# Performance work log

Hardware: AMD Instinct MI355X
Metric: run time of the kernel (lower is better)

The kernel has to match this reference:

```python
import jax, jax.numpy as jnp
import numpy as np

TOP_K = 2
NORM_TOPK_PROB = True


def setup_inputs() -> dict:
    key = jax.random.key(0)
    k1, k2, k3, k4 = jax.random.split(key, 4)
    B, S, H = 1, 1024, 2048
    E, I = 16, 768
    hidden_states = jax.random.normal(k1, (B, S, H), dtype=jnp.float32)
    # 0.02 init scale keeps router logits / activations in a realistic range
    gate_w = jax.random.normal(k2, (E, H), dtype=jnp.float32) * 0.02
    w1 = jax.random.normal(k3, (E, 2 * I, H), dtype=jnp.float32) * 0.02  # [gate; up] stacked
    w2 = jax.random.normal(k4, (E, H, I), dtype=jnp.float32) * 0.02
    return {"hidden_states": hidden_states, "gate_w": gate_w, "w1": w1, "w2": w2}


def reference(hidden_states, gate_w, w1, w2):
    B, S, H = hidden_states.shape
    E = gate_w.shape[0]
    I = w2.shape[2]
    x = hidden_states.reshape(-1, H)  # [T, H]

    # Router
    router_logits = x @ gate_w.T  # [T, E]
    probs = jax.nn.softmax(router_logits.astype(jnp.float32), axis=-1)
    topk_w, topk_ids = jax.lax.top_k(probs, TOP_K)  # [T, K]
    if NORM_TOPK_PROB:
        topk_w = topk_w / jnp.sum(topk_w, axis=-1, keepdims=True)
    topk_w = topk_w.astype(x.dtype)

    # combine[t, e] = sum_k topk_w[t, k] * 1[topk_ids[t, k] == e]
    combine = jnp.sum(jax.nn.one_hot(topk_ids, E, dtype=x.dtype) * topk_w[..., None], axis=1)  # [T, E]

    def expert(w1_e, w2_e):
        h = x @ w1_e.T                      # [T, 2I]
        act = jax.nn.silu(h[:, :I]) * h[:, I:]  # fused SiLU-and-mul
        return act @ w2_e.T                 # [T, H]

    y_all = jax.vmap(expert)(w1, w2)        # [E, T, H]
    out = jnp.einsum('te,eth->th', combine, y_all)  # weighted scatter-sum over experts
    return out, router_logits
```

## Files before the change

### kernel.cpp

```cpp
#include <hip/hip_runtime.h>
#include <hip/hip_bf16.h>


#define T_TOK 1024
#define HDIM  2048
#define NEXP  16
#define IDIM  768
#define CAP   192
#define BK    64

typedef __attribute__((ext_vector_type(8))) short  short8_t;
typedef __attribute__((ext_vector_type(4))) float  f32x4_t;

static __device__ __forceinline__ unsigned short f2bf(float f) {
  unsigned u = __float_as_uint(f);
  u += 0x7FFFu + ((u >> 16) & 1u);
  return (unsigned short)(u >> 16);
}
static __device__ __forceinline__ float bf2f(unsigned short h) {
  return __uint_as_float(((unsigned)h) << 16);
}
static __device__ __forceinline__ void cvt_store4(unsigned short* dst, float4 v) {
  ushort4 u;
  u.x = f2bf(v.x); u.y = f2bf(v.y); u.z = f2bf(v.z); u.w = f2bf(v.w);
  *(ushort4*)dst = u;
}

__global__ __launch_bounds__(256) void moe_router(
    const float* __restrict__ x, const float* __restrict__ gw,
    float* __restrict__ logits_out, int* __restrict__ cnt,
    int* __restrict__ tok, float* __restrict__ wl) {
  const int t = blockIdx.x;
  const int tid = threadIdx.x;
  const int lane = tid & 63, wid = tid >> 6;
  const float4* xv = (const float4*)(x + (size_t)t * HDIM);
  float4 v0 = xv[tid * 2], v1 = xv[tid * 2 + 1];
  float acc[NEXP];
#pragma unroll
  for (int e = 0; e < NEXP; ++e) {
    const float4* gv = (const float4*)(gw + (size_t)e * HDIM);
    float4 g0 = gv[tid * 2], g1 = gv[tid * 2 + 1];
    acc[e] = v0.x * g0.x + v0.y * g0.y + v0.z * g0.z + v0.w * g0.w +
             v1.x * g1.x + v1.y * g1.y + v1.z * g1.z + v1.w * g1.w;
  }
#pragma unroll
  for (int e = 0; e < NEXP; ++e)
#pragma unroll
    for (int off = 32; off; off >>= 1) acc[e] += __shfl_xor(acc[e], off, 64);
  __shared__ float red[4][NEXP];
  if (lane == 0)
#pragma unroll
    for (int e = 0; e < NEXP; ++e) red[wid][e] = acc[e];
  __syncthreads();
  if (tid < NEXP) {
    float s = red[0][tid] + red[1][tid] + red[2][tid] + red[3][tid];
    logits_out[(size_t)t * NEXP + tid] = s;
    red[0][tid] = s;
  }
  __syncthreads();
  if (tid == 0) {
    int e1 = -1, e2 = -1;
    float l1 = -1e30f, l2 = -1e30f;
#pragma unroll
    for (int e = 0; e < NEXP; ++e) {
      float v = red[0][e];
      if (v > l1)      { l2 = l1; e2 = e1; l1 = v; e1 = e; }
      else if (v > l2) { l2 = v;  e2 = e; }
    }
    float wa = 1.f / (1.f + __expf(l2 - l1));
    float wb = 1.f - wa;
    int p1 = atomicAdd(&cnt[e1], 1);
    if (p1 < CAP) { tok[e1 * CAP + p1] = t; wl[e1 * CAP + p1] = wa; }
    int p2 = atomicAdd(&cnt[e2], 1);
    if (p2 < CAP) { tok[e2 * CAP + p2] = t; wl[e2 * CAP + p2] = wb; }
  }
}

__global__ __launch_bounds__(256, 3) void moe_stage_a(
    const float* __restrict__ x, const float* __restrict__ w1,
    const int* __restrict__ cnt, const int* __restrict__ tok,
    unsigned short* __restrict__ h_ws) {
  int bx = blockIdx.x;
  const int ks = bx & 1; bx >>= 1;
  const int mt = bx & 1; bx >>= 1;
  const int nt = bx % 24;
  const int e  = bx / 24;
  int ne = cnt[e]; if (ne > CAP) ne = CAP;
  if (mt * 128 >= ne) return;

  __shared__ unsigned short As[128][BK + 8];
  __shared__ unsigned short Bs[64][BK + 8];
  __shared__ int toks[128];
  const int tid = threadIdx.x;
  if (tid < 128) {
    int idx = mt * 128 + tid;
    toks[tid] = tok[e * CAP + (idx < ne ? idx : 0)];
  }
  __syncthreads();

  const int k0 = ks * (HDIM / 2);
  const float* aB[8];
#pragma unroll
  for (int i = 0; i < 8; ++i) {
    int c = tid + 256 * i, r = c >> 4, c4 = c & 15;
    aB[i] = x + (size_t)toks[r] * HDIM + k0 + c4 * 4;
  }
  const float* w1e = w1 + ((size_t)e * (2 * IDIM) + nt * 64) * HDIM + k0;
  const float* bB[4];
#pragma unroll
  for (int i = 0; i < 4; ++i) {
    int c = tid + 256 * i, r = c >> 4, c4 = c & 15;
    bB[i] = w1e + (size_t)r * HDIM + c4 * 4;
  }

  float4 aR[8], bR[4];
#pragma unroll
  for (int i = 0; i < 8; ++i) aR[i] = *(const float4*)(aB[i]);
#pragma unroll
  for (int i = 0; i < 4; ++i) bR[i] = *(const float4*)(bB[i]);

  const int lane = tid & 63, wv = tid >> 6;
  const int wr = wv >> 1, wc = wv & 1;
  const int quad = lane >> 4, lr = lane & 15;
  f32x4_t acc[4][2] = {};

  for (int kk = 0; kk < HDIM / 2; kk += BK) {
#pragma unroll
    for (int i = 0; i < 8; ++i) {
      int c = tid + 256 * i;
      cvt_store4(&As[c >> 4][(c & 15) * 4], aR[i]);
    }
#pragma unroll
    for (int i = 0; i < 4; ++i) {
      int c = tid + 256 * i;
      cvt_store4(&Bs[c >> 4][(c & 15) * 4], bR[i]);
    }
    __syncthreads();
    if (kk + BK < HDIM / 2) {
      int kn = kk + BK;
#pragma unroll
      for (int i = 0; i < 8; ++i) aR[i] = *(const float4*)(aB[i] + kn);
#pragma unroll
      for (int i = 0; i < 4; ++i) bR[i] = *(const float4*)(bB[i] + kn);
    }
    short8_t a[2][4], b[2][2];
#pragma unroll
    for (int k2 = 0; k2 < 2; ++k2) {
#pragma unroll
      for (int i = 0; i < 4; ++i)
        a[k2][i] = *(const short8_t*)&As[wr * 64 + i * 16 + lr][k2 * 32 + quad * 8];
#pragma unroll
      for (int j = 0; j < 2; ++j)
        b[k2][j] = *(const short8_t*)&Bs[wc * 32 + j * 16 + lr][k2 * 32 + quad * 8];
    }
#pragma unroll
    for (int k2 = 0; k2 < 2; ++k2)
#pragma unroll
      for (int i = 0; i < 4; ++i)
#pragma unroll
        for (int j = 0; j < 2; ++j)
          acc[i][j] = __builtin_amdgcn_mfma_f32_16x16x32_bf16(
              a[k2][i], b[k2][j], acc[i][j], 0, 0, 0);
    __syncthreads();
  }

  unsigned short* hp = h_ws + ((size_t)ks * NEXP + e) * CAP * (2 * IDIM);
#pragma unroll
  for (int i = 0; i < 4; ++i) {
    int mb = mt * 128 + wr * 64 + i * 16;
    if (mb >= CAP) continue;
#pragma unroll
    for (int j = 0; j < 2; ++j) {
      int ng = nt * 64 + wc * 32 + j * 16 + lr;
#pragma unroll
      for (int rr = 0; rr < 4; ++rr) {
        int mg = mb + quad * 4 + rr;
        hp[(size_t)mg * (2 * IDIM) + ng] = f2bf(acc[i][j][rr]);
      }
    }
  }
}

__global__ __launch_bounds__(256) void moe_merge(
    const unsigned short* __restrict__ h_ws, unsigned short* __restrict__ act) {
  const size_t half = (size_t)NEXP * CAP * (2 * IDIM);
  int c = blockIdx.x * 256 + threadIdx.x;
  int row = c / (IDIM / 4);
  int c4  = c % (IDIM / 4);
  size_t gb = (size_t)row * (2 * IDIM) + c4 * 4;
  ushort4 g0 = *(const ushort4*)(h_ws + gb);
  ushort4 g1 = *(const ushort4*)(h_ws + half + gb);
  ushort4 u0 = *(const ushort4*)(h_ws + gb + IDIM);
  ushort4 u1 = *(const ushort4*)(h_ws + half + gb + IDIM);
  float g, u;
  ushort4 o;
  g = bf2f(g0.x) + bf2f(g1.x); u = bf2f(u0.x) + bf2f(u1.x);
  o.x = f2bf(g / (1.f + __expf(-g)) * u);
  g = bf2f(g0.y) + bf2f(g1.y); u = bf2f(u0.y) + bf2f(u1.y);
  o.y = f2bf(g / (1.f + __expf(-g)) * u);
  g = bf2f(g0.z) + bf2f(g1.z); u = bf2f(u0.z) + bf2f(u1.z);
  o.z = f2bf(g / (1.f + __expf(-g)) * u);
  g = bf2f(g0.w) + bf2f(g1.w); u = bf2f(u0.w) + bf2f(u1.w);
  o.w = f2bf(g / (1.f + __expf(-g)) * u);
  *(ushort4*)(act + (size_t)row * IDIM + c4 * 4) = o;
}

__global__ __launch_bounds__(256, 2) void moe_stage_b(
    const unsigned short* __restrict__ act, const float* __restrict__ w2,
    const int* __restrict__ cnt, const int* __restrict__ tok,
    const float* __restrict__ wl, float* __restrict__ out) {
  int bx = blockIdx.x;
  const int mt = bx & 1; bx >>= 1;
  const int nt = bx & 31;
  const int e  = bx >> 5;
  int ne = cnt[e]; if (ne > CAP) ne = CAP;
  if (mt * 128 >= ne) return;

  __shared__ unsigned short As[128][BK + 8];
  __shared__ unsigned short Bs[64][BK + 8];
  __shared__ int   toks[128];
  __shared__ float wts[128];
  const int tid = threadIdx.x;
  if (tid < 128) {
    int idx = mt * 128 + tid;
    bool v = idx < ne;
    toks[tid] = tok[e * CAP + (v ? idx : 0)];
    wts[tid]  = v ? wl[e * CAP + idx] : 0.f;
  }
  __syncthreads();

  const unsigned short* actb = act + ((size_t)e * CAP + mt * 128) * IDIM;
  const unsigned short* aB[8];
#pragma unroll
  for (int i = 0; i < 8; ++i) {
    int c = tid + 256 * i, r = c >> 4, c4 = c & 15;
    aB[i] = actb + (size_t)r * IDIM + c4 * 4;
  }
  const float* w2e = w2 + ((size_t)e * HDIM + nt * 64) * IDIM;
  const float* bB[4];
#pragma unroll
  for (int i = 0; i < 4; ++i) {
    int c = tid + 256 * i, r = c >> 4, c4 = c & 15;
    bB[i] = w2e + (size_t)r * IDIM + c4 * 4;
  }

  ushort4 aR[8]; float4 bR[4];
#pragma unroll
  for (int i = 0; i < 8; ++i) aR[i] = *(const ushort4*)(aB[i]);
#pragma unroll
  for (int i = 0; i < 4; ++i) bR[i] = *(const float4*)(bB[i]);

  const int lane = tid & 63, wv = tid >> 6;
  const int wr = wv >> 1, wc = wv & 1;
  const int quad = lane >> 4, lr = lane & 15;
  f32x4_t acc[4][2] = {};

  for (int kk = 0; kk < IDIM; kk += BK) {
#pragma unroll
    for (int i = 0; i < 8; ++i) {
      int c = tid + 256 * i;
      *(ushort4*)&As[c >> 4][(c & 15) * 4] = aR[i];
    }
#pragma unroll
    for (int i = 0; i < 4; ++i) {
      int c = tid + 256 * i;
      cvt_store4(&Bs[c >> 4][(c & 15) * 4], bR[i]);
    }
    __syncthreads();
    if (kk + BK < IDIM) {
      int kn = kk + BK;
#pragma unroll
      for (int i = 0; i < 8; ++i) aR[i] = *(const ushort4*)(aB[i] + kn);
#pragma unroll
      for (int i = 0; i < 4; ++i) bR[i] = *(const float4*)(bB[i] + kn);
    }
    short8_t a[2][4], b[2][2];
#pragma unroll
    for (int k2 = 0; k2 < 2; ++k2) {
#pragma unroll
      for (int i = 0; i < 4; ++i)
        a[k2][i] = *(const short8_t*)&As[wr * 64 + i * 16 + lr][k2 * 32 + quad * 8];
#pragma unroll
      for (int j = 0; j < 2; ++j)
        b[k2][j] = *(const short8_t*)&Bs[wc * 32 + j * 16 + lr][k2 * 32 + quad * 8];
    }
#pragma unroll
    for (int k2 = 0; k2 < 2; ++k2)
#pragma unroll
      for (int i = 0; i < 4; ++i)
#pragma unroll
        for (int j = 0; j < 2; ++j)
          acc[i][j] = __builtin_amdgcn_mfma_f32_16x16x32_bf16(
              a[k2][i], b[k2][j], acc[i][j], 0, 0, 0);
    __syncthreads();
  }

#pragma unroll
  for (int i = 0; i < 4; ++i) {
#pragma unroll
    for (int j = 0; j < 2; ++j) {
      int ng = nt * 64 + wc * 32 + j * 16 + lr;
#pragma unroll
      for (int rr = 0; rr < 4; ++rr) {
        int ml = wr * 64 + i * 16 + quad * 4 + rr;
        atomicAdd(&out[(size_t)toks[ml] * HDIM + ng], acc[i][j][rr] * wts[ml]);
      }
    }
  }
}

extern "C" void kernel_launch(void* const* d_in, const int* in_sizes, int n_in,
                              void* d_out, int out_size, void* d_ws,
                              size_t ws_size, hipStream_t stream) {
  (void)in_sizes; (void)n_in; (void)out_size; (void)ws_size;
  const float* x  = (const float*)d_in[0];
  const float* gw = (const float*)d_in[1];
  const float* w1 = (const float*)d_in[2];
  const float* w2 = (const float*)d_in[3];
  float* out    = (float*)d_out;
  float* logits = out + (size_t)T_TOK * HDIM;

  char* ws = (char*)d_ws;
  int*   cnt = (int*)ws;
  int*   tok = (int*)(ws + 256);
  float* wl  = (float*)(ws + 256 + NEXP * CAP * 4);
  unsigned short* act =
      (unsigned short*)(ws + 25088);
  unsigned short* h_ws =
      (unsigned short*)(ws + 25088 + (size_t)NEXP * CAP * IDIM * 2);

  hipMemsetAsync(cnt, 0, 256, stream);
  hipMemsetAsync(d_out, 0, (size_t)T_TOK * HDIM * sizeof(float), stream);

  moe_router <<<T_TOK, 256, 0, stream>>>(x, gw, logits, cnt, tok, wl);
  moe_stage_a<<<NEXP * 24 * 2 * 2, 256, 0, stream>>>(x, w1, cnt, tok, h_ws);
  moe_merge  <<<NEXP * CAP * IDIM / 4 / 256, 256, 0, stream>>>(h_ws, act);
  moe_stage_b<<<NEXP * 32 * 2, 256, 0, stream>>>(act, w2, cnt, tok, wl, out);
}
```

Baseline: 489.1 us.

## Pre-convert x to bf16, add split-K to both stages, shrink K tile

A new kernel converts x to bf16 once, so stage A no longer loads and converts fp32 activations inside its inner loop. Stage A split-K grows to 4 when the workspace allows it, and the merge kernel sums a variable number of partials. Stage B gains a 2-way split-K that relies on its existing atomic accumulation. Both GEMMs drop to a 32-wide K tile with occupancy hint 4, giving more blocks and fewer registers, at the cost of more barriers, more partial-sum traffic and more atomics.

```diff
diff --git a/kernel.cpp b/kernel.cpp
--- a/kernel.cpp
+++ b/kernel.cpp
@@ -7,7 +7,6 @@
 #define NEXP  16
 #define IDIM  768
 #define CAP   192
-#define BK    64
 
 typedef __attribute__((ext_vector_type(8))) short  short8_t;
 typedef __attribute__((ext_vector_type(4))) float  f32x4_t;
@@ -24,6 +23,13 @@
   ushort4 u;
   u.x = f2bf(v.x); u.y = f2bf(v.y); u.z = f2bf(v.z); u.w = f2bf(v.w);
   *(ushort4*)dst = u;
+}
+
+__global__ __launch_bounds__(256) void cvt_x(
+    const float* __restrict__ x, unsigned short* __restrict__ xb) {
+  int i = blockIdx.x * 256 + threadIdx.x;
+  float4 v = ((const float4*)x)[i];
+  cvt_store4(xb + (size_t)i * 4, v);
 }
 
 __global__ __launch_bounds__(256) void moe_router(
@@ -76,20 +82,20 @@
   }
 }
 
-__global__ __launch_bounds__(256, 3) void moe_stage_a(
-    const float* __restrict__ x, const float* __restrict__ w1,
+__global__ __launch_bounds__(256, 4) void moe_stage_a(
+    const unsigned short* __restrict__ xb, const float* __restrict__ w1,
     const int* __restrict__ cnt, const int* __restrict__ tok,
-    unsigned short* __restrict__ h_ws) {
+    unsigned short* __restrict__ h_ws, int ksa, int kchunk) {
   int bx = blockIdx.x;
-  const int ks = bx & 1; bx >>= 1;
+  const int ks = bx % ksa; bx /= ksa;
   const int mt = bx & 1; bx >>= 1;
   const int nt = bx % 24;
   const int e  = bx / 24;
   int ne = cnt[e]; if (ne > CAP) ne = CAP;
   if (mt * 128 >= ne) return;
 
-  __shared__ unsigned short As[128][BK + 8];
-  __shared__ unsigned short Bs[64][BK + 8];
+  __shared__ unsigned short As[128][40];
+  __shared__ unsigned short Bs[64][40];
   __shared__ int toks[128];
   const int tid = threadIdx.x;
   if (tid < 128) {
@@ -98,69 +104,57 @@
   }
   __syncthreads();
 
-  const int k0 = ks * (HDIM / 2);
-  const float* aB[8];
-#pragma unroll
-  for (int i = 0; i < 8; ++i) {
-    int c = tid + 256 * i, r = c >> 4, c4 = c & 15;
-    aB[i] = x + (size_t)toks[r] * HDIM + k0 + c4 * 4;
+  const int k0 = ks * kchunk;
+  const unsigned short* aB[2];
+  int ar[2], ag[2], br[2], bc[2];
+#pragma unroll
+  for (int i = 0; i < 2; ++i) {
+    int c = tid + 256 * i;
+    ar[i] = c >> 2; ag[i] = c & 3;
+    aB[i] = xb + (size_t)toks[ar[i]] * HDIM + k0 + ag[i] * 8;
+    br[i] = c >> 3; bc[i] = c & 7;
   }
   const float* w1e = w1 + ((size_t)e * (2 * IDIM) + nt * 64) * HDIM + k0;
-  const float* bB[4];
-#pragma unroll
-  for (int i = 0; i < 4; ++i) {
-    int c = tid + 256 * i, r = c >> 4, c4 = c & 15;
-    bB[i] = w1e + (size_t)r * HDIM + c4 * 4;
-  }
-
-  float4 aR[8], bR[4];
-#pragma unroll
-  for (int i = 0; i < 8; ++i) aR[i] = *(const float4*)(aB[i]);
-#pragma unroll
-  for (int i = 0; i < 4; ++i) bR[i] = *(const float4*)(bB[i]);
+  const float* bB[2];
+#pragma unroll
+  for (int i = 0; i < 2; ++i) bB[i] = w1e + (size_t)br[i] * HDIM + bc[i] * 4;
+
+  short8_t aR[2]; float4 bR[2];
+#pragma unroll
+  for (int i = 0; i < 2; ++i) aR[i] = *(const short8_t*)(aB[i]);
+#pragma unroll
+  for (int i = 0; i < 2; ++i) bR[i] = *(const float4*)(bB[i]);
 
   const int lane = tid & 63, wv = tid >> 6;
   const int wr = wv >> 1, wc = wv & 1;
   const int quad = lane >> 4, lr = lane & 15;
   f32x4_t acc[4][2] = {};
 
-  for (int kk = 0; kk < HDIM / 2; kk += BK) {
-#pragma unroll
-    for (int i = 0; i < 8; ++i) {
-      int c = tid + 256 * i;
-      cvt_store4(&As[c >> 4][(c & 15) * 4], aR[i]);
-    }
-#pragma unroll
-    for (int i = 0; i < 4; ++i) {
-      int c = tid + 256 * i;
-      cvt_store4(&Bs[c >> 4][(c & 15) * 4], bR[i]);
-    }
+  for (int kk = 0; kk < kchunk; kk += 32) {
+#pragma unroll
+    for (int i = 0; i < 2; ++i) *(short8_t*)&As[ar[i]][ag[i] * 8] = aR[i];
+#pragma unroll
+    for (int i = 0; i < 2; ++i) cvt_store4(&Bs[br[i]][bc[i] * 4], bR[i]);
     __syncthreads();
-    if (kk + BK < HDIM / 2) {
-      int kn = kk + BK;
-#pragma unroll
-      for (int i = 0; i < 8; ++i) aR[i] = *(const float4*)(aB[i] + kn);
-#pragma unroll
-      for (int i = 0; i < 4; ++i) bR[i] = *(const float4*)(bB[i] + kn);
-    }
-    short8_t a[2][4], b[2][2];
-#pragma unroll
-    for (int k2 = 0; k2 < 2; ++k2) {
-#pragma unroll
-      for (int i = 0; i < 4; ++i)
-        a[k2][i] = *(const short8_t*)&As[wr * 64 + i * 16 + lr][k2 * 32 + quad * 8];
+    if (kk + 32 < kchunk) {
+#pragma unroll
+      for (int i = 0; i < 2; ++i) aR[i] = *(const short8_t*)(aB[i] + kk + 32);
+#pragma unroll
+      for (int i = 0; i < 2; ++i) bR[i] = *(const float4*)(bB[i] + kk + 32);
+    }
+    short8_t a[4], b[2];
+#pragma unroll
+    for (int i = 0; i < 4; ++i)
+      a[i] = *(const short8_t*)&As[wr * 64 + i * 16 + lr][quad * 8];
+#pragma unroll
+    for (int j = 0; j < 2; ++j)
+      b[j] = *(const short8_t*)&Bs[wc * 32 + j * 16 + lr][quad * 8];
+#pragma unroll
+    for (int i = 0; i < 4; ++i)
 #pragma unroll
       for (int j = 0; j < 2; ++j)
-        b[k2][j] = *(const short8_t*)&Bs[wc * 32 + j * 16 + lr][k2 * 32 + quad * 8];
-    }
-#pragma unroll
-    for (int k2 = 0; k2 < 2; ++k2)
-#pragma unroll
-      for (int i = 0; i < 4; ++i)
-#pragma unroll
-        for (int j = 0; j < 2; ++j)
-          acc[i][j] = __builtin_amdgcn_mfma_f32_16x16x32_bf16(
-              a[k2][i], b[k2][j], acc[i][j], 0, 0, 0);
+        acc[i][j] = __builtin_amdgcn_mfma_f32_16x16x32_bf16(
+            a[i], b[j], acc[i][j], 0, 0, 0);
     __syncthreads();
   }
 
@@ -182,42 +176,42 @@
 }
 
 __global__ __launch_bounds__(256) void moe_merge(
-    const unsigned short* __restrict__ h_ws, unsigned short* __restrict__ act) {
-  const size_t half = (size_t)NEXP * CAP * (2 * IDIM);
+    const unsigned short* __restrict__ h_ws, unsigned short* __restrict__ act,
+    int ksa) {
+  const size_t part = (size_t)NEXP * CAP * (2 * IDIM);
   int c = blockIdx.x * 256 + threadIdx.x;
   int row = c / (IDIM / 4);
   int c4  = c % (IDIM / 4);
   size_t gb = (size_t)row * (2 * IDIM) + c4 * 4;
-  ushort4 g0 = *(const ushort4*)(h_ws + gb);
-  ushort4 g1 = *(const ushort4*)(h_ws + half + gb);
-  ushort4 u0 = *(const ushort4*)(h_ws + gb + IDIM);
-  ushort4 u1 = *(const ushort4*)(h_ws + half + gb + IDIM);
-  float g, u;
+  float g[4] = {0.f, 0.f, 0.f, 0.f}, u[4] = {0.f, 0.f, 0.f, 0.f};
+  for (int s = 0; s < ksa; ++s) {
+    ushort4 gs = *(const ushort4*)(h_ws + (size_t)s * part + gb);
+    ushort4 us = *(const ushort4*)(h_ws + (size_t)s * part + gb + IDIM);
+    g[0] += bf2f(gs.x); g[1] += bf2f(gs.y); g[2] += bf2f(gs.z); g[3] += bf2f(gs.w);
+    u[0] += bf2f(us.x); u[1] += bf2f(us.y); u[2] += bf2f(us.z); u[3] += bf2f(us.w);
+  }
   ushort4 o;
-  g = bf2f(g0.x) + bf2f(g1.x); u = bf2f(u0.x) + bf2f(u1.x);
-  o.x = f2bf(g / (1.f + __expf(-g)) * u);
-  g = bf2f(g0.y) + bf2f(g1.y); u = bf2f(u0.y) + bf2f(u1.y);
-  o.y = f2bf(g / (1.f + __expf(-g)) * u);
-  g = bf2f(g0.z) + bf2f(g1.z); u = bf2f(u0.z) + bf2f(u1.z);
-  o.z = f2bf(g / (1.f + __expf(-g)) * u);
-  g = bf2f(g0.w) + bf2f(g1.w); u = bf2f(u0.w) + bf2f(u1.w);
-  o.w = f2bf(g / (1.f + __expf(-g)) * u);
+  o.x = f2bf(g[0] / (1.f + __expf(-g[0])) * u[0]);
+  o.y = f2bf(g[1] / (1.f + __expf(-g[1])) * u[1]);
+  o.z = f2bf(g[2] / (1.f + __expf(-g[2])) * u[2]);
+  o.w = f2bf(g[3] / (1.f + __expf(-g[3])) * u[3]);
   *(ushort4*)(act + (size_t)row * IDIM + c4 * 4) = o;
 }
 
-__global__ __launch_bounds__(256, 2) void moe_stage_b(
+__global__ __launch_bounds__(256, 4) void moe_stage_b(
     const unsigned short* __restrict__ act, const float* __restrict__ w2,
     const int* __restrict__ cnt, const int* __restrict__ tok,
     const float* __restrict__ wl, float* __restrict__ out) {
   int bx = blockIdx.x;
-  const int mt = bx & 1; bx >>= 1;
-  const int nt = bx & 31;
-  const int e  = bx >> 5;
+  const int ks = bx & 1;
+  const int mt = (bx >> 1) & 1;
+  const int nt = (bx >> 2) & 31;
+  const int e  = bx >> 7;
   int ne = cnt[e]; if (ne > CAP) ne = CAP;
   if (mt * 128 >= ne) return;
 
-  __shared__ unsigned short As[128][BK + 8];
-  __shared__ unsigned short Bs[64][BK + 8];
+  __shared__ unsigned short As[128][40];
+  __shared__ unsigned short Bs[64][40];
   __shared__ int   toks[128];
   __shared__ float wts[128];
   const int tid = threadIdx.x;
@@ -229,69 +223,57 @@
   }
   __syncthreads();
 
-  const unsigned short* actb = act + ((size_t)e * CAP + mt * 128) * IDIM;
-  const unsigned short* aB[8];
-#pragma unroll
-  for (int i = 0; i < 8; ++i) {
-    int c = tid + 256 * i, r = c >> 4, c4 = c & 15;
-    aB[i] = actb + (size_t)r * IDIM + c4 * 4;
-  }
-  const float* w2e = w2 + ((size_t)e * HDIM + nt * 64) * IDIM;
-  const float* bB[4];
-#pragma unroll
-  for (int i = 0; i < 4; ++i) {
-    int c = tid + 256 * i, r = c >> 4, c4 = c & 15;
-    bB[i] = w2e + (size_t)r * IDIM + c4 * 4;
-  }
-
-  ushort4 aR[8]; float4 bR[4];
-#pragma unroll
-  for (int i = 0; i < 8; ++i) aR[i] = *(const ushort4*)(aB[i]);
-#pragma unroll
-  for (int i = 0; i < 4; ++i) bR[i] = *(const float4*)(bB[i]);
+  const int k0 = ks * (IDIM / 2);
+  const unsigned short* actb = act + ((size_t)e * CAP + mt * 128) * IDIM + k0;
+  const float* w2e = w2 + ((size_t)e * HDIM + nt * 64) * IDIM + k0;
+  const unsigned short* aB[2];
+  const float* bB[2];
+  int ar[2], ag[2], br[2], bc[2];
+#pragma unroll
+  for (int i = 0; i < 2; ++i) {
+    int c = tid + 256 * i;
+    ar[i] = c >> 2; ag[i] = c & 3;
+    aB[i] = actb + (size_t)ar[i] * IDIM + ag[i] * 8;
+    br[i] = c >> 3; bc[i] = c & 7;
+    bB[i] = w2e + (size_t)br[i] * IDIM + bc[i] * 4;
+  }
+
+  short8_t aR[2]; float4 bR[2];
+#pragma unroll
+  for (int i = 0; i < 2; ++i) aR[i] = *(const short8_t*)(aB[i]);
+#pragma unroll
+  for (int i = 0; i < 2; ++i) bR[i] = *(const float4*)(bB[i]);
 
   const int lane = tid & 63, wv = tid >> 6;
   const int wr = wv >> 1, wc = wv & 1;
   const int quad = lane >> 4, lr = lane & 15;
   f32x4_t acc[4][2] = {};
 
-  for (int kk = 0; kk < IDIM; kk += BK) {
-#pragma unroll
-    for (int i = 0; i < 8; ++i) {
-      int c = tid + 256 * i;
-      *(ushort4*)&As[c >> 4][(c & 15) * 4] = aR[i];
-    }
-#pragma unroll
-    for (int i = 0; i < 4; ++i) {
-      int c = tid + 256 * i;
-      cvt_store4(&Bs[c >> 4][(c & 15) * 4], bR[i]);
-    }
+  for (int kk = 0; kk < IDIM / 2; kk += 32) {
+#pragma unroll
+    for (int i = 0; i < 2; ++i) *(short8_t*)&As[ar[i]][ag[i] * 8] = aR[i];
+#pragma unroll
+    for (int i = 0; i < 2; ++i) cvt_store4(&Bs[br[i]][bc[i] * 4], bR[i]);
     __syncthreads();
-    if (kk + BK < IDIM) {
-      int kn = kk + BK;
-#pragma unroll
-      for (int i = 0; i < 8; ++i) aR[i] = *(const ushort4*)(aB[i] + kn);
-#pragma unroll
-      for (int i = 0; i < 4; ++i) bR[i] = *(const float4*)(bB[i] + kn);
-    }
-    short8_t a[2][4], b[2][2];
-#pragma unroll
-    for (int k2 = 0; k2 < 2; ++k2) {
-#pragma unroll
-      for (int i = 0; i < 4; ++i)
-        a[k2][i] = *(const short8_t*)&As[wr * 64 + i * 16 + lr][k2 * 32 + quad * 8];
+    if (kk + 32 < IDIM / 2) {
+#pragma unroll
+      for (int i = 0; i < 2; ++i) aR[i] = *(const short8_t*)(aB[i] + kk + 32);
+#pragma unroll
+      for (int i = 0; i < 2; ++i) bR[i] = *(const float4*)(bB[i] + kk + 32);
+    }
+    short8_t a[4], b[2];
+#pragma unroll
+    for (int i = 0; i < 4; ++i)
+      a[i] = *(const short8_t*)&As[wr * 64 + i * 16 + lr][quad * 8];
+#pragma unroll
+    for (int j = 0; j < 2; ++j)
+      b[j] = *(const short8_t*)&Bs[wc * 32 + j * 16 + lr][quad * 8];
+#pragma unroll
+    for (int i = 0; i < 4; ++i)
 #pragma unroll
       for (int j = 0; j < 2; ++j)
-        b[k2][j] = *(const short8_t*)&Bs[wc * 32 + j * 16 + lr][k2 * 32 + quad * 8];
-    }
-#pragma unroll
-    for (int k2 = 0; k2 < 2; ++k2)
-#pragma unroll
-      for (int i = 0; i < 4; ++i)
-#pragma unroll
-        for (int j = 0; j < 2; ++j)
-          acc[i][j] = __builtin_amdgcn_mfma_f32_16x16x32_bf16(
-              a[k2][i], b[k2][j], acc[i][j], 0, 0, 0);
+        acc[i][j] = __builtin_amdgcn_mfma_f32_16x16x32_bf16(
+            a[i], b[j], acc[i][j], 0, 0, 0);
     __syncthreads();
   }
 
@@ -312,7 +294,7 @@
 extern "C" void kernel_launch(void* const* d_in, const int* in_sizes, int n_in,
                               void* d_out, int out_size, void* d_ws,
                               size_t ws_size, hipStream_t stream) {
-  (void)in_sizes; (void)n_in; (void)out_size; (void)ws_size;
+  (void)in_sizes; (void)n_in; (void)out_size;
   const float* x  = (const float*)d_in[0];
   const float* gw = (const float*)d_in[1];
   const float* w1 = (const float*)d_in[2];
@@ -324,16 +306,22 @@
   int*   cnt = (int*)ws;
   int*   tok = (int*)(ws + 256);
   float* wl  = (float*)(ws + 256 + NEXP * CAP * 4);
-  unsigned short* act =
-      (unsigned short*)(ws + 25088);
-  unsigned short* h_ws =
-      (unsigned short*)(ws + 25088 + (size_t)NEXP * CAP * IDIM * 2);
+  unsigned short* xb  = (unsigned short*)(ws + 25088);
+  unsigned short* act = xb;
+  unsigned short* h_ws = (unsigned short*)(ws + 25088 + (size_t)NEXP * CAP * IDIM * 2);
+
+  const size_t part_b = (size_t)NEXP * CAP * 2 * IDIM * 2;
+  const size_t base   = 25088 + (size_t)NEXP * CAP * IDIM * 2;
+  const int ksa = (ws_size >= base + 4 * part_b) ? 4 : 2;
+  const int kchunk = HDIM / ksa;
 
   hipMemsetAsync(cnt, 0, 256, stream);
   hipMemsetAsync(d_out, 0, (size_t)T_TOK * HDIM * sizeof(float), stream);
 
+  cvt_x      <<<T_TOK * HDIM / 4 / 256, 256, 0, stream>>>(x, xb);
   moe_router <<<T_TOK, 256, 0, stream>>>(x, gw, logits, cnt, tok, wl);
-  moe_stage_a<<<NEXP * 24 * 2 * 2, 256, 0, stream>>>(x, w1, cnt, tok, h_ws);
-  moe_merge  <<<NEXP * CAP * IDIM / 4 / 256, 256, 0, stream>>>(h_ws, act);
-  moe_stage_b<<<NEXP * 32 * 2, 256, 0, stream>>>(act, w2, cnt, tok, wl, out);
-}
+  moe_stage_a<<<NEXP * 24 * 2 * ksa, 256, 0, stream>>>(
+      xb, w1, cnt, tok, h_ws, ksa, kchunk);
+  moe_merge  <<<NEXP * CAP * IDIM / 4 / 256, 256, 0, stream>>>(h_ws, act, ksa);
+  moe_stage_b<<<NEXP * 32 * 2 * 2, 256, 0, stream>>>(act, w2, cnt, tok, wl, out);
+}
```

Result: slower. 592.3 us (+21.1%).

## Replace LDS-tiled MoE GEMMs with per-wave register-fed MFMA tiles

Applied to the files above, without the earlier changes.

Both expert GEMM stages are restructured so each wave independently computes a 128x32 tile. MFMA fragments are loaded straight from global memory with a register double buffer, which removes the shared-memory staging and block barriers. A new pre-pass converts the activations to bf16 once. Stage B gains a split-K of 2 using atomic accumulation, and weights are now truncated to bf16 instead of rounded. In exchange, L2 sees more redundant weight and activation traffic, atomics roughly double, and the truncation adds a small precision loss.

```diff
diff --git a/kernel.cpp b/kernel.cpp
--- a/kernel.cpp
+++ b/kernel.cpp
@@ -7,7 +7,6 @@
 #define NEXP  16
 #define IDIM  768
 #define CAP   192
-#define BK    64
 
 typedef __attribute__((ext_vector_type(8))) short  short8_t;
 typedef __attribute__((ext_vector_type(4))) float  f32x4_t;
@@ -17,6 +16,9 @@
   u += 0x7FFFu + ((u >> 16) & 1u);
   return (unsigned short)(u >> 16);
 }
+static __device__ __forceinline__ short f2bf_t(float f) {
+  return (short)(__float_as_uint(f) >> 16);
+}
 static __device__ __forceinline__ float bf2f(unsigned short h) {
   return __uint_as_float(((unsigned)h) << 16);
 }
@@ -24,6 +26,19 @@
   ushort4 u;
   u.x = f2bf(v.x); u.y = f2bf(v.y); u.z = f2bf(v.z); u.w = f2bf(v.w);
   *(ushort4*)dst = u;
+}
+static __device__ __forceinline__ short8_t pack_bf16(float4 lo, float4 hi) {
+  short8_t r;
+  r[0] = f2bf_t(lo.x); r[1] = f2bf_t(lo.y); r[2] = f2bf_t(lo.z); r[3] = f2bf_t(lo.w);
+  r[4] = f2bf_t(hi.x); r[5] = f2bf_t(hi.y); r[6] = f2bf_t(hi.z); r[7] = f2bf_t(hi.w);
+  return r;
+}
+
+__global__ __launch_bounds__(256) void cvt_x(
+    const float* __restrict__ x, unsigned short* __restrict__ xb) {
+  int i = blockIdx.x * 256 + threadIdx.x;
+  float4 v = ((const float4*)x)[i];
+  cvt_store4(xb + (size_t)i * 4, v);
 }
 
 __global__ __launch_bounds__(256) void moe_router(
@@ -76,106 +91,86 @@
   }
 }
 
-__global__ __launch_bounds__(256, 3) void moe_stage_a(
-    const float* __restrict__ x, const float* __restrict__ w1,
+__global__ __launch_bounds__(256, 2) void moe_stage_a(
+    const unsigned short* __restrict__ xb, const float* __restrict__ w1,
     const int* __restrict__ cnt, const int* __restrict__ tok,
     unsigned short* __restrict__ h_ws) {
-  int bx = blockIdx.x;
-  const int ks = bx & 1; bx >>= 1;
-  const int mt = bx & 1; bx >>= 1;
-  const int nt = bx % 24;
-  const int e  = bx / 24;
+  int gid = blockIdx.x * 4 + (threadIdx.x >> 6);
+  const int ks = gid & 1; gid >>= 1;
+  const int mt = gid & 1; gid >>= 1;
+  const int nt = gid % 48;
+  const int e  = gid / 48;
   int ne = cnt[e]; if (ne > CAP) ne = CAP;
   if (mt * 128 >= ne) return;
 
-  __shared__ unsigned short As[128][BK + 8];
-  __shared__ unsigned short Bs[64][BK + 8];
-  __shared__ int toks[128];
-  const int tid = threadIdx.x;
-  if (tid < 128) {
-    int idx = mt * 128 + tid;
-    toks[tid] = tok[e * CAP + (idx < ne ? idx : 0)];
-  }
-  __syncthreads();
-
-  const int k0 = ks * (HDIM / 2);
-  const float* aB[8];
-#pragma unroll
-  for (int i = 0; i < 8; ++i) {
-    int c = tid + 256 * i, r = c >> 4, c4 = c & 15;
-    aB[i] = x + (size_t)toks[r] * HDIM + k0 + c4 * 4;
-  }
-  const float* w1e = w1 + ((size_t)e * (2 * IDIM) + nt * 64) * HDIM + k0;
-  const float* bB[4];
-#pragma unroll
-  for (int i = 0; i < 4; ++i) {
-    int c = tid + 256 * i, r = c >> 4, c4 = c & 15;
-    bB[i] = w1e + (size_t)r * HDIM + c4 * 4;
-  }
-
-  float4 aR[8], bR[4];
-#pragma unroll
-  for (int i = 0; i < 8; ++i) aR[i] = *(const float4*)(aB[i]);
-#pragma unroll
-  for (int i = 0; i < 4; ++i) bR[i] = *(const float4*)(bB[i]);
-
-  const int lane = tid & 63, wv = tid >> 6;
-  const int wr = wv >> 1, wc = wv & 1;
-  const int quad = lane >> 4, lr = lane & 15;
-  f32x4_t acc[4][2] = {};
-
-  for (int kk = 0; kk < HDIM / 2; kk += BK) {
-#pragma unroll
-    for (int i = 0; i < 8; ++i) {
-      int c = tid + 256 * i;
-      cvt_store4(&As[c >> 4][(c & 15) * 4], aR[i]);
-    }
-#pragma unroll
-    for (int i = 0; i < 4; ++i) {
-      int c = tid + 256 * i;
-      cvt_store4(&Bs[c >> 4][(c & 15) * 4], bR[i]);
-    }
-    __syncthreads();
-    if (kk + BK < HDIM / 2) {
-      int kn = kk + BK;
-#pragma unroll
-      for (int i = 0; i < 8; ++i) aR[i] = *(const float4*)(aB[i] + kn);
-#pragma unroll
-      for (int i = 0; i < 4; ++i) bR[i] = *(const float4*)(bB[i] + kn);
-    }
-    short8_t a[2][4], b[2][2];
-#pragma unroll
-    for (int k2 = 0; k2 < 2; ++k2) {
-#pragma unroll
-      for (int i = 0; i < 4; ++i)
-        a[k2][i] = *(const short8_t*)&As[wr * 64 + i * 16 + lr][k2 * 32 + quad * 8];
-#pragma unroll
-      for (int j = 0; j < 2; ++j)
-        b[k2][j] = *(const short8_t*)&Bs[wc * 32 + j * 16 + lr][k2 * 32 + quad * 8];
-    }
-#pragma unroll
-    for (int k2 = 0; k2 < 2; ++k2)
-#pragma unroll
-      for (int i = 0; i < 4; ++i)
-#pragma unroll
-        for (int j = 0; j < 2; ++j)
-          acc[i][j] = __builtin_amdgcn_mfma_f32_16x16x32_bf16(
-              a[k2][i], b[k2][j], acc[i][j], 0, 0, 0);
-    __syncthreads();
-  }
-
-  unsigned short* hp = h_ws + ((size_t)ks * NEXP + e) * CAP * (2 * IDIM);
-#pragma unroll
-  for (int i = 0; i < 4; ++i) {
-    int mb = mt * 128 + wr * 64 + i * 16;
-    if (mb >= CAP) continue;
-#pragma unroll
-    for (int j = 0; j < 2; ++j) {
-      int ng = nt * 64 + wc * 32 + j * 16 + lr;
-#pragma unroll
-      for (int rr = 0; rr < 4; ++rr) {
-        int mg = mb + quad * 4 + rr;
-        hp[(size_t)mg * (2 * IDIM) + ng] = f2bf(acc[i][j][rr]);
+  const int lane = threadIdx.x & 63;
+  const int lr = lane & 15, quad = lane >> 4;
+
+  const unsigned short* aP[8];
+#pragma unroll
+  for (int mi = 0; mi < 8; ++mi) {
+    int slot = mt * 128 + mi * 16 + lr;
+    int sc = slot < ne ? slot : ne - 1;
+    aP[mi] = xb + (size_t)tok[e * CAP + sc] * HDIM + ks * 1024 + quad * 8;
+  }
+  const float* bP[2];
+#pragma unroll
+  for (int nj = 0; nj < 2; ++nj)
+    bP[nj] = w1 + ((size_t)e * (2 * IDIM) + nt * 32 + nj * 16 + lr) * HDIM +
+             ks * 1024 + quad * 8;
+
+  short8_t aC[8]; float4 bC[2][2];
+#pragma unroll
+  for (int mi = 0; mi < 8; ++mi) aC[mi] = *(const short8_t*)(aP[mi]);
+#pragma unroll
+  for (int nj = 0; nj < 2; ++nj) {
+    bC[nj][0] = *(const float4*)(bP[nj]);
+    bC[nj][1] = *(const float4*)(bP[nj] + 4);
+  }
+
+  f32x4_t acc[8][2] = {};
+  for (int k = 0; k < 1024; k += 32) {
+    short8_t aN[8]; float4 bN[2][2];
+    const bool more = (k + 32) < 1024;
+    if (more) {
+#pragma unroll
+      for (int mi = 0; mi < 8; ++mi)
+        aN[mi] = *(const short8_t*)(aP[mi] + k + 32);
+#pragma unroll
+      for (int nj = 0; nj < 2; ++nj) {
+        bN[nj][0] = *(const float4*)(bP[nj] + k + 32);
+        bN[nj][1] = *(const float4*)(bP[nj] + k + 36);
+      }
+    }
+    short8_t bh[2];
+#pragma unroll
+    for (int nj = 0; nj < 2; ++nj) bh[nj] = pack_bf16(bC[nj][0], bC[nj][1]);
+#pragma unroll
+    for (int mi = 0; mi < 8; ++mi)
+#pragma unroll
+      for (int nj = 0; nj < 2; ++nj)
+        acc[mi][nj] = __builtin_amdgcn_mfma_f32_16x16x32_bf16(
+            aC[mi], bh[nj], acc[mi][nj], 0, 0, 0);
+    if (more) {
+#pragma unroll
+      for (int mi = 0; mi < 8; ++mi) aC[mi] = aN[mi];
+#pragma unroll
+      for (int nj = 0; nj < 2; ++nj) { bC[nj][0] = bN[nj][0]; bC[nj][1] = bN[nj][1]; }
+    }
+  }
+
+  unsigned short* hp = h_ws + (size_t)ks * NEXP * CAP * (2 * IDIM) +
+                       (size_t)e * CAP * (2 * IDIM);
+#pragma unroll
+  for (int mi = 0; mi < 8; ++mi) {
+#pragma unroll
+    for (int r = 0; r < 4; ++r) {
+      int slot = mt * 128 + mi * 16 + quad * 4 + r;
+      if (slot < CAP) {
+#pragma unroll
+        for (int nj = 0; nj < 2; ++nj)
+          hp[(size_t)slot * (2 * IDIM) + nt * 32 + nj * 16 + lr] =
+              f2bf(acc[mi][nj][r]);
       }
     }
   }
@@ -183,17 +178,16 @@
 
 __global__ __launch_bounds__(256) void moe_merge(
     const unsigned short* __restrict__ h_ws, unsigned short* __restrict__ act) {
-  const size_t half = (size_t)NEXP * CAP * (2 * IDIM);
+  const size_t part = (size_t)NEXP * CAP * (2 * IDIM);
   int c = blockIdx.x * 256 + threadIdx.x;
   int row = c / (IDIM / 4);
   int c4  = c % (IDIM / 4);
   size_t gb = (size_t)row * (2 * IDIM) + c4 * 4;
   ushort4 g0 = *(const ushort4*)(h_ws + gb);
-  ushort4 g1 = *(const ushort4*)(h_ws + half + gb);
+  ushort4 g1 = *(const ushort4*)(h_ws + part + gb);
   ushort4 u0 = *(const ushort4*)(h_ws + gb + IDIM);
-  ushort4 u1 = *(const ushort4*)(h_ws + half + gb + IDIM);
-  float g, u;
-  ushort4 o;
+  ushort4 u1 = *(const ushort4*)(h_ws + part + gb + IDIM);
+  float g, u; ushort4 o;
   g = bf2f(g0.x) + bf2f(g1.x); u = bf2f(u0.x) + bf2f(u1.x);
   o.x = f2bf(g / (1.f + __expf(-g)) * u);
   g = bf2f(g0.y) + bf2f(g1.y); u = bf2f(u0.y) + bf2f(u1.y);
@@ -209,101 +203,82 @@
     const unsigned short* __restrict__ act, const float* __restrict__ w2,
     const int* __restrict__ cnt, const int* __restrict__ tok,
     const float* __restrict__ wl, float* __restrict__ out) {
-  int bx = blockIdx.x;
-  const int mt = bx & 1; bx >>= 1;
-  const int nt = bx & 31;
-  const int e  = bx >> 5;
+  int gid = blockIdx.x * 4 + (threadIdx.x >> 6);
+  const int ks = gid & 1;
+  const int mt = (gid >> 1) & 1;
+  const int nt = (gid >> 2) & 63;
+  const int e  = gid >> 8;
   int ne = cnt[e]; if (ne > CAP) ne = CAP;
   if (mt * 128 >= ne) return;
 
-  __shared__ unsigned short As[128][BK + 8];
-  __shared__ unsigned short Bs[64][BK + 8];
-  __shared__ int   toks[128];
-  __shared__ float wts[128];
-  const int tid = threadIdx.x;
-  if (tid < 128) {
-    int idx = mt * 128 + tid;
-    bool v = idx < ne;
-    toks[tid] = tok[e * CAP + (v ? idx : 0)];
-    wts[tid]  = v ? wl[e * CAP + idx] : 0.f;
-  }
-  __syncthreads();
-
-  const unsigned short* actb = act + ((size_t)e * CAP + mt * 128) * IDIM;
-  const unsigned short* aB[8];
-#pragma unroll
-  for (int i = 0; i < 8; ++i) {
-    int c = tid + 256 * i, r = c >> 4, c4 = c & 15;
-    aB[i] = actb + (size_t)r * IDIM + c4 * 4;
-  }
-  const float* w2e = w2 + ((size_t)e * HDIM + nt * 64) * IDIM;
-  const float* bB[4];
-#pragma unroll
-  for (int i = 0; i < 4; ++i) {
-    int c = tid + 256 * i, r = c >> 4, c4 = c & 15;
-    bB[i] = w2e + (size_t)r * IDIM + c4 * 4;
-  }
-
-  ushort4 aR[8]; float4 bR[4];
-#pragma unroll
-  for (int i = 0; i < 8; ++i) aR[i] = *(const ushort4*)(aB[i]);
-#pragma unroll
-  for (int i = 0; i < 4; ++i) bR[i] = *(const float4*)(bB[i]);
-
-  const int lane = tid & 63, wv = tid >> 6;
-  const int wr = wv >> 1, wc = wv & 1;
-  const int quad = lane >> 4, lr = lane & 15;
-  f32x4_t acc[4][2] = {};
-
-  for (int kk = 0; kk < IDIM; kk += BK) {
-#pragma unroll
-    for (int i = 0; i < 8; ++i) {
-      int c = tid + 256 * i;
-      *(ushort4*)&As[c >> 4][(c & 15) * 4] = aR[i];
-    }
-#pragma unroll
-    for (int i = 0; i < 4; ++i) {
-      int c = tid + 256 * i;
-      cvt_store4(&Bs[c >> 4][(c & 15) * 4], bR[i]);
-    }
-    __syncthreads();
-    if (kk + BK < IDIM) {
-      int kn = kk + BK;
-#pragma unroll
-      for (int i = 0; i < 8; ++i) aR[i] = *(const ushort4*)(aB[i] + kn);
-#pragma unroll
-      for (int i = 0; i < 4; ++i) bR[i] = *(const float4*)(bB[i] + kn);
-    }
-    short8_t a[2][4], b[2][2];
-#pragma unroll
-    for (int k2 = 0; k2 < 2; ++k2) {
-#pragma unroll
-      for (int i = 0; i < 4; ++i)
-        a[k2][i] = *(const short8_t*)&As[wr * 64 + i * 16 + lr][k2 * 32 + quad * 8];
-#pragma unroll
-      for (int j = 0; j < 2; ++j)
-        b[k2][j] = *(const short8_t*)&Bs[wc * 32 + j * 16 + lr][k2 * 32 + quad * 8];
-    }
-#pragma unroll
-    for (int k2 = 0; k2 < 2; ++k2)
-#pragma unroll
-      for (int i = 0; i < 4; ++i)
-#pragma unroll
-        for (int j = 0; j < 2; ++j)
-          acc[i][j] = __builtin_amdgcn_mfma_f32_16x16x32_bf16(
-              a[k2][i], b[k2][j], acc[i][j], 0, 0, 0);
-    __syncthreads();
-  }
-
-#pragma unroll
-  for (int i = 0; i < 4; ++i) {
-#pragma unroll
-    for (int j = 0; j < 2; ++j) {
-      int ng = nt * 64 + wc * 32 + j * 16 + lr;
-#pragma unroll
-      for (int rr = 0; rr < 4; ++rr) {
-        int ml = wr * 64 + i * 16 + quad * 4 + rr;
-        atomicAdd(&out[(size_t)toks[ml] * HDIM + ng], acc[i][j][rr] * wts[ml]);
+  const int lane = threadIdx.x & 63;
+  const int lr = lane & 15, quad = lane >> 4;
+
+  const unsigned short* aP[8];
+#pragma unroll
+  for (int mi = 0; mi < 8; ++mi) {
+    int slot = mt * 128 + mi * 16 + lr;
+    int sc = slot < CAP ? slot : CAP - 1;
+    aP[mi] = act + ((size_t)e * CAP + sc) * IDIM + ks * 384 + quad * 8;
+  }
+  const float* bP[2];
+#pragma unroll
+  for (int nj = 0; nj < 2; ++nj)
+    bP[nj] = w2 + ((size_t)e * HDIM + nt * 32 + nj * 16 + lr) * IDIM +
+             ks * 384 + quad * 8;
+
+  short8_t aC[8]; float4 bC[2][2];
+#pragma unroll
+  for (int mi = 0; mi < 8; ++mi) aC[mi] = *(const short8_t*)(aP[mi]);
+#pragma unroll
+  for (int nj = 0; nj < 2; ++nj) {
+    bC[nj][0] = *(const float4*)(bP[nj]);
+    bC[nj][1] = *(const float4*)(bP[nj] + 4);
+  }
+
+  f32x4_t acc[8][2] = {};
+  for (int k = 0; k < 384; k += 32) {
+    short8_t aN[8]; float4 bN[2][2];
+    const bool more = (k + 32) < 384;
+    if (more) {
+#pragma unroll
+      for (int mi = 0; mi < 8; ++mi)
+        aN[mi] = *(const short8_t*)(aP[mi] + k + 32);
+#pragma unroll
+      for (int nj = 0; nj < 2; ++nj) {
+        bN[nj][0] = *(const float4*)(bP[nj] + k + 32);
+        bN[nj][1] = *(const float4*)(bP[nj] + k + 36);
+      }
+    }
+    short8_t bh[2];
+#pragma unroll
+    for (int nj = 0; nj < 2; ++nj) bh[nj] = pack_bf16(bC[nj][0], bC[nj][1]);
+#pragma unroll
+    for (int mi = 0; mi < 8; ++mi)
+#pragma unroll
+      for (int nj = 0; nj < 2; ++nj)
+        acc[mi][nj] = __builtin_amdgcn_mfma_f32_16x16x32_bf16(
+            aC[mi], bh[nj], acc[mi][nj], 0, 0, 0);
+    if (more) {
+#pragma unroll
+      for (int mi = 0; mi < 8; ++mi) aC[mi] = aN[mi];
+#pragma unroll
+      for (int nj = 0; nj < 2; ++nj) { bC[nj][0] = bN[nj][0]; bC[nj][1] = bN[nj][1]; }
+    }
+  }
+
+#pragma unroll
+  for (int mi = 0; mi < 8; ++mi) {
+#pragma unroll
+    for (int r = 0; r < 4; ++r) {
+      int slot = mt * 128 + mi * 16 + quad * 4 + r;
+      if (slot < ne) {
+        float w = wl[e * CAP + slot];
+        int   t = tok[e * CAP + slot];
+#pragma unroll
+        for (int nj = 0; nj < 2; ++nj)
+          atomicAdd(&out[(size_t)t * HDIM + nt * 32 + nj * 16 + lr],
+                    acc[mi][nj][r] * w);
       }
     }
   }
@@ -324,16 +299,17 @@
   int*   cnt = (int*)ws;
   int*   tok = (int*)(ws + 256);
   float* wl  = (float*)(ws + 256 + NEXP * CAP * 4);
-  unsigned short* act =
-      (unsigned short*)(ws + 25088);
+  unsigned short* xb  = (unsigned short*)(ws + 24832);
+  unsigned short* act = xb;
   unsigned short* h_ws =
-      (unsigned short*)(ws + 25088 + (size_t)NEXP * CAP * IDIM * 2);
+      (unsigned short*)(ws + 24832 + (size_t)NEXP * CAP * IDIM * 2);
 
   hipMemsetAsync(cnt, 0, 256, stream);
   hipMemsetAsync(d_out, 0, (size_t)T_TOK * HDIM * sizeof(float), stream);
 
+  cvt_x      <<<T_TOK * HDIM / 4 / 256, 256, 0, stream>>>(x, xb);
   moe_router <<<T_TOK, 256, 0, stream>>>(x, gw, logits, cnt, tok, wl);
-  moe_stage_a<<<NEXP * 24 * 2 * 2, 256, 0, stream>>>(x, w1, cnt, tok, h_ws);
+  moe_stage_a<<<NEXP * 48 * 2 * 2 / 4, 256, 0, stream>>>(xb, w1, cnt, tok, h_ws);
   moe_merge  <<<NEXP * CAP * IDIM / 4 / 256, 256, 0, stream>>>(h_ws, act);
-  moe_stage_b<<<NEXP * 32 * 2, 256, 0, stream>>>(act, w2, cnt, tok, wl, out);
-}
+  moe_stage_b<<<NEXP * 64 * 2 * 2 / 4, 256, 0, stream>>>(act, w2, cnt, tok, wl, out);
+}
```

Result: slower. 542.7 us (+11.0%).
